# Optimization experiments

Hardware: AMD Instinct MI355X
Metric: run time of the kernel (lower is better)

Reference implementation:

```python
import jax, jax.numpy as jnp
import numpy as np

EPS = 1e-5      # BatchNorm eps (eval mode, running stats at init: mean=0, var=1)
SLOPE = 0.2     # LeakyReLU negative slope


def _knn_idx(x, k):
    # x: (B, N, D) -> (B, N, k) indices of k nearest neighbors (squared L2, feature space)
    sq = jnp.sum(x * x, axis=-1)                              # (B, N)
    dist = sq[:, :, None] + sq[:, None, :] - 2.0 * jnp.einsum('bnd,bmd->bnm', x, x)
    return jax.lax.top_k(-dist, k)[1]                         # nearest = largest of -dist


def _bn_lrelu(y, gamma, beta):
    # eval BatchNorm with running_mean=0, running_var=1, then LeakyReLU(0.2)
    y = y * (gamma / jnp.sqrt(1.0 + EPS)) + beta
    return jnp.where(y >= 0, y, SLOPE * y)


def _edge_conv(x, W, gamma, beta, k):
    # x: (B, N, D); W: (C_out, 2D). Returns (B, N, C_out) after max over k neighbors.
    idx = _knn_idx(x, k)                                      # (B, N, k)
    nb = jax.vmap(lambda xt, i: xt[i])(x, idx)                # (B, N, k, D) neighbor gather
    ctr = jnp.broadcast_to(x[:, :, None, :], nb.shape)
    feat = jnp.concatenate([nb - ctr, ctr], axis=-1)          # (B, N, k, 2D)
    y = jnp.einsum('bnkd,od->bnko', feat, W)                  # 1x1 conv (no bias)
    y = _bn_lrelu(y, gamma, beta)
    return jnp.max(y, axis=2)                                 # max-pool over neighbors


def setup_inputs() -> dict:
    key = jax.random.key(0)
    ks = jax.random.split(key, 16)
    B, N, k, out_dim = 8, 4096, 20, 512
    x = jax.random.normal(ks[0], (B, 3, N), dtype=jnp.float32)
    dims = [(64, 6), (64, 128), (128, 128), (256, 256), (out_dim, 512)]
    inp = {'x': x, 'k': k}
    for i, (co, ci) in enumerate(dims, start=1):
        inp[f'W{i}'] = jax.random.normal(ks[3 * i - 2], (co, ci), dtype=jnp.float32) * (1.0 / np.sqrt(ci))
        inp[f'g{i}'] = jax.random.uniform(ks[3 * i - 1], (co,), dtype=jnp.float32, minval=0.5, maxval=1.5)
        inp[f'b{i}'] = 0.1 * jax.random.normal(ks[3 * i], (co,), dtype=jnp.float32)
    return inp


def reference(x, W1, g1, b1, W2, g2, b2, W3, g3, b3, W4, g4, b4, W5, g5, b5, k):
    xt = jnp.transpose(x, (0, 2, 1))                          # (B, N, 3)
    x1 = _edge_conv(xt, W1, g1, b1, k)                        # (B, N, 64)
    x2 = _edge_conv(x1, W2, g2, b2, k)                        # (B, N, 64)
    x3 = _edge_conv(x2, W3, g3, b3, k)                        # (B, N, 128)
    x4 = _edge_conv(x3, W4, g4, b4, k)                        # (B, N, 256)
    h = jnp.concatenate([x1, x2, x3, x4], axis=-1)            # (B, N, 512)
    y = _bn_lrelu(jnp.einsum('bnd,od->bno', h, W5), g5, b5)   # (B, N, out_dim)
    return jnp.concatenate([jnp.max(y, axis=1), jnp.mean(y, axis=1)], axis=-1)  # (B, 2*out_dim)
```

## Files before the change

### kernel.cpp

```cpp
#include <hip/hip_runtime.h>
#include <math.h>

#define BATCH 8
#define N_PTS 4096
#define KNN 20
#define EPS_BN 1e-5f
#define SLOPE 0.2f
#define M_ROWS (BATCH * N_PTS)

typedef __attribute__((ext_vector_type(8))) short short8;
typedef __attribute__((ext_vector_type(2))) float float2v;
typedef __attribute__((ext_vector_type(4))) float float4v;
typedef __attribute__((ext_vector_type(16))) float float16v;

__device__ __forceinline__ unsigned short f2bf(float f) {
    unsigned u = __float_as_uint(f);
    unsigned r = (u + 0x7FFFu + ((u >> 16) & 1u)) >> 16;
    return (unsigned short)r;
}
__device__ __forceinline__ float bf2f(unsigned short h) {
    return __uint_as_float((unsigned)h << 16);
}

__global__ void convert_x1(const float* __restrict__ x,
                           unsigned short* __restrict__ xh, unsigned short* __restrict__ xl,
                           float* __restrict__ sq) {
    int i = blockIdx.x * blockDim.x + threadIdx.x;
    if (i >= M_ROWS) return;
    int b = i / N_PTS, n = i % N_PTS;
    float v[3], s = 0.f;
    #pragma unroll
    for (int d = 0; d < 3; ++d) {
        v[d] = x[((size_t)b * 3 + d) * N_PTS + n];
        s += v[d] * v[d];
    }
    sq[i] = s;
    #pragma unroll
    for (int d = 0; d < 32; ++d) {
        float f = (d < 3) ? v[d] : 0.f;
        unsigned short h = f2bf(f);
        xh[(size_t)i * 32 + d] = h;
        xl[(size_t)i * 32 + d] = f2bf(f - bf2f(h));
    }
}

__global__ void sqnorm_hl(const unsigned short* __restrict__ hh,
                          const unsigned short* __restrict__ hl,
                          int D, float* __restrict__ sq) {
    int w = threadIdx.x >> 6, lane = threadIdx.x & 63;
    int row = blockIdx.x * 4 + w;
    if (row >= M_ROWS) return;
    const unsigned short* ph = hh + (size_t)row * 512;
    const unsigned short* pl = hl + (size_t)row * 512;
    float s = 0.f;
    for (int d = lane; d < D; d += 64) {
        float v = bf2f(ph[d]) + bf2f(pl[d]);
        s += v * v;
    }
    #pragma unroll
    for (int off = 32; off > 0; off >>= 1) s += __shfl_down(s, off, 64);
    if (lane == 0) sq[row] = s;
}

__global__ void repack_edge_split(const float* __restrict__ W, int Co, int D, int KP,
                                  unsigned short* __restrict__ Wh, unsigned short* __restrict__ Wl) {
    int i = blockIdx.x * blockDim.x + threadIdx.x;
    int tot = 2 * Co * KP;
    if (i >= tot) return;
    int r = i / KP, d = i % KP;
    float v = 0.f;
    if (d < D) v = (r < Co) ? W[(size_t)r * 2 * D + d] : W[(size_t)(r - Co) * 2 * D + D + d];
    unsigned short h = f2bf(v);
    Wh[i] = h; Wl[i] = f2bf(v - bf2f(h));
}

__global__ void repack_w5_split(const float* __restrict__ W,
                                unsigned short* __restrict__ Wh, unsigned short* __restrict__ Wl) {
    int i = blockIdx.x * blockDim.x + threadIdx.x;
    if (i >= 512 * 512) return;
    float v = W[i];
    unsigned short h = f2bf(v);
    Wh[i] = h; Wl[i] = f2bf(v - bf2f(h));
}

template<int DPAD>
__launch_bounds__(DPAD >= 128 ? 256 : 512, 2)
__global__ void knn_mfma(const unsigned short* __restrict__ Xh,
                         const unsigned short* __restrict__ Xl,
                         int strideX,
                         const float* __restrict__ sq, int* __restrict__ idxout) {
    constexpr int KS16 = DPAD / 16;
    constexpr int NW   = (DPAD >= 128) ? 4 : 8;
    constexpr int NCH  = NW / 4;
    constexpr int CHR  = N_PTS / NCH;
    constexpr int SST  = 34;
    constexpr size_t SFB   = (size_t)NW * 32 * SST * 4;
    constexpr size_t THR   = (size_t)NW * 64 * 4;
    constexpr size_t MERGE = (size_t)64 * NW * KNN * 4 + (size_t)64 * NW * KNN * 2;
    constexpr size_t POOL  = (SFB + THR) > MERGE ? (SFB + THR) : MERGE;
    __shared__ __align__(16) char smem[POOL];
    float* Sfw  = (float*)smem + (size_t)(threadIdx.x >> 6) * 32 * SST;
    float* thrT = (float*)(smem + SFB);
    float*          kb   = (float*)smem;
    unsigned short* ib16 = (unsigned short*)(kb + 64 * NW * KNN);

    const int b = blockIdx.y;
    const int row0 = blockIdx.x * 64;
    const int tid = threadIdx.x;
    const int w = tid >> 6, lane = tid & 63;
    const int l31 = lane & 31, lh = lane >> 5;
    const int rbase = (w & 1) * 32;
    const int cb32  = ((w >> 1) & 1) * 32;
    const int chalf = w >> 2;
    const int cs    = chalf * CHR;
    const int rowb  = rbase + l31;
    const int slot  = ((w >> 1) & 1) * 2 + lh + chalf * 4;

    const unsigned short* Xhb = Xh + (size_t)b * N_PTS * strideX;
    const unsigned short* Xlb = Xl + (size_t)b * N_PTS * strideX;
    const float* sqb = sq + (size_t)b * N_PTS;

    short8 ah[KS16], al[KS16];
    #pragma unroll
    for (int ks = 0; ks < KS16; ++ks) {
        size_t o = (size_t)(row0 + rbase + l31) * strideX + ks * 16 + lh * 8;
        ah[ks] = *(const short8*)(Xhb + o);
        al[ks] = *(const short8*)(Xlb + o);
    }

    const unsigned short* pBh = Xhb + (size_t)(cb32 + l31) * strideX + lh * 8;
    const unsigned short* pBl = Xlb + (size_t)(cb32 + l31) * strideX + lh * 8;
    const float* psq = sqb + cb32 + l31;

    float fv[KNN]; int fi[KNN];
    #pragma unroll
    for (int p = 0; p < KNN; ++p) { fv[p] = INFINITY; fi[p] = 0x7FFFFFFF; }

    thrT[tid] = INFINITY;
    __syncthreads();

    #pragma unroll 1
    for (int c0 = cs; c0 < cs + CHR; c0 += 64) {
        short8 bh[KS16], bl[KS16];
        #pragma unroll
        for (int ks = 0; ks < KS16; ++ks) {
            bh[ks] = *(const short8*)(pBh + (size_t)c0 * strideX + ks * 16);
            bl[ks] = *(const short8*)(pBl + (size_t)c0 * strideX + ks * 16);
        }
        float sc = psq[c0];

        float16v a0 = {}, a1 = {}, a2 = {};
        #pragma unroll
        for (int ks = 0; ks < KS16; ++ks) {
            if (KS16 <= 4) {
                a0 = __builtin_amdgcn_mfma_f32_32x32x16_bf16(ah[ks], bh[ks], a0, 0, 0, 0);
                a1 = __builtin_amdgcn_mfma_f32_32x32x16_bf16(al[ks], bh[ks], a1, 0, 0, 0);
                a2 = __builtin_amdgcn_mfma_f32_32x32x16_bf16(ah[ks], bl[ks], a2, 0, 0, 0);
            } else {
                a0 = __builtin_amdgcn_mfma_f32_32x32x16_bf16(ah[ks], bh[ks], a0, 0, 0, 0);
                a1 = __builtin_amdgcn_mfma_f32_32x32x16_bf16(al[ks], bh[ks], a1, 0, 0, 0);
                a0 = __builtin_amdgcn_mfma_f32_32x32x16_bf16(ah[ks], bl[ks], a0, 0, 0, 0);
            }
        }

        #pragma unroll
        for (int reg = 0; reg < 16; ++reg) {
            int rowL = (reg & 3) + 8 * (reg >> 2) + 4 * lh;
            float acv = (KS16 <= 4) ? (a0[reg] + a1[reg] + a2[reg]) : (a0[reg] + a1[reg]);
            Sfw[rowL * SST + l31] = sc - 2.f * acv;
        }
        asm volatile("s_waitcnt lgkmcnt(0)" ::: "memory");

        float fT = thrT[rowb];
        #pragma unroll
        for (int s = 1; s < NW; ++s) fT = fminf(fT, thrT[s * 64 + rowb]);
        float f19 = fv[KNN - 1];

        const int sbase = l31 * SST + lh * 16;
        float2v c2[8];
        #pragma unroll
        for (int u = 0; u < 8; ++u) c2[u] = *(const float2v*)&Sfw[sbase + 2 * u];
        unsigned mask = 0;
        #pragma unroll
        for (int u = 0; u < 8; ++u) {
            if (c2[u][0] < f19 && c2[u][0] <= fT) mask |= (1u << (2 * u));
            if (c2[u][1] < f19 && c2[u][1] <= fT) mask |= (1u << (2 * u + 1));
        }

        const int cidx = c0 + cb32 + lh * 16;
        while (mask) {
            int jj = __ffs(mask) - 1;
            mask &= mask - 1;
            bool j1 = jj & 1, j2 = jj & 2, j4 = jj & 4, j8 = jj & 8;
            float t0 = j1 ? c2[0][1] : c2[0][0];
            float t1 = j1 ? c2[1][1] : c2[1][0];
            float t2 = j1 ? c2[2][1] : c2[2][0];
            float t3 = j1 ? c2[3][1] : c2[3][0];
            float t4 = j1 ? c2[4][1] : c2[4][0];
            float t5 = j1 ? c2[5][1] : c2[5][0];
            float t6 = j1 ? c2[6][1] : c2[6][0];
            float t7 = j1 ? c2[7][1] : c2[7][0];
            float u0 = j2 ? t1 : t0;
            float u1 = j2 ? t3 : t2;
            float u2 = j2 ? t5 : t4;
            float u3 = j2 ? t7 : t6;
            float r0 = j4 ? u1 : u0;
            float r1 = j4 ? u3 : u2;
            float v  = j8 ? r1 : r0;
            if (v < fv[KNN - 1]) {
                fv[KNN - 1] = v;
                fi[KNN - 1] = cidx + jj;
                #pragma unroll
                for (int p = KNN - 1; p > 0; --p) {
                    float va = fv[p - 1], vb = fv[p];
                    int   ia = fi[p - 1], ic = fi[p];
                    bool sw = vb < va;
                    fv[p - 1] = sw ? vb : va; fv[p] = sw ? va : vb;
                    fi[p - 1] = sw ? ic : ia; fi[p] = sw ? ia : ic;
                }
            }
        }

        thrT[slot * 64 + rowb] = fv[KNN - 1];
    }

    __syncthreads();
    {
        int base = (rowb * NW + slot) * KNN;
        #pragma unroll
        for (int p = 0; p < KNN; ++p) {
            kb[base + p] = fv[p];
            ib16[base + p] = (unsigned short)fi[p];
        }
    }
    __syncthreads();

    if constexpr (NW == 8) {
        if (tid < 128) {
            int row = tid & 63, half = tid >> 6;
            int base = (row * 8 + half * 4) * KNN;
            #pragma unroll
            for (int p = 0; p < KNN; ++p) { fv[p] = kb[base + p]; fi[p] = (int)ib16[base + p]; }
            #pragma unroll 1
            for (int qq = 0; qq < 3 * KNN; ++qq) {
                float v  = kb[base + KNN + qq];
                int   ii = (int)ib16[base + KNN + qq];
                bool ins = (v < fv[KNN - 1]) ||
                           (v == fv[KNN - 1] && ii < fi[KNN - 1]);
                if (ins) {
                    fv[KNN - 1] = v; fi[KNN - 1] = ii;
                    #pragma unroll
                    for (int p = KNN - 1; p > 0; --p) {
                        float va = fv[p - 1], vb = fv[p];
                        int   ia = fi[p - 1], ic = fi[p];
                        bool sw = (vb < va) || (vb == va && ic < ia);
                        fv[p - 1] = sw ? vb : va; fv[p] = sw ? va : vb;
                        fi[p - 1] = sw ? ic : ia; fi[p] = sw ? ia : ic;
                    }
                }
            }
            if (half == 1) {
                int ob = (row * 8 + 4) * KNN;
                #pragma unroll
                for (int p = 0; p < KNN; ++p) {
                    kb[ob + p] = fv[p]; ib16[ob + p] = (unsigned short)fi[p];
                }
            }
        }
        __syncthreads();
        if (tid < 64) {
            int base = (tid * 8 + 4) * KNN;
            #pragma unroll 1
            for (int qq = 0; qq < KNN; ++qq) {
                float v  = kb[base + qq];
                int   ii = (int)ib16[base + qq];
                bool ins = (v < fv[KNN - 1]) ||
                           (v == fv[KNN - 1] && ii < fi[KNN - 1]);
                if (ins) {
                    fv[KNN - 1] = v; fi[KNN - 1] = ii;
                    #pragma unroll
                    for (int p = KNN - 1; p > 0; --p) {
                        float va = fv[p - 1], vb = fv[p];
                        int   ia = fi[p - 1], ic = fi[p];
                        bool sw = (vb < va) || (vb == va && ic < ia);
                        fv[p - 1] = sw ? vb : va; fv[p] = sw ? va : vb;
                        fi[p - 1] = sw ? ic : ia; fi[p] = sw ? ia : ic;
                    }
                }
            }
            int* op = idxout + ((size_t)(b * N_PTS + row0 + tid)) * KNN;
            #pragma unroll
            for (int p = 0; p < KNN; ++p) op[p] = fi[p];
        }
    } else {
        if (tid < 64) {
            int base = tid * 4 * KNN;
            #pragma unroll
            for (int p = 0; p < KNN; ++p) { fv[p] = kb[base + p]; fi[p] = (int)ib16[base + p]; }
            #pragma unroll 1
            for (int qq = 0; qq < 3 * KNN; ++qq) {
                float v  = kb[base + KNN + qq];
                int   ii = (int)ib16[base + KNN + qq];
                bool ins = (v < fv[KNN - 1]) ||
                           (v == fv[KNN - 1] && ii < fi[KNN - 1]);
                if (ins) {
                    fv[KNN - 1] = v; fi[KNN - 1] = ii;
                    #pragma unroll
                    for (int p = KNN - 1; p > 0; --p) {
                        float va = fv[p - 1], vb = fv[p];
                        int   ia = fi[p - 1], ic = fi[p];
                        bool sw = (vb < va) || (vb == va && ic < ia);
                        fv[p - 1] = sw ? vb : va; fv[p] = sw ? va : vb;
                        fi[p - 1] = sw ? ic : ia; fi[p] = sw ? ia : ic;
                    }
                }
            }
            int* op = idxout + ((size_t)(b * N_PTS + row0 + tid)) * KNN;
            #pragma unroll
            for (int p = 0; p < KNN; ++p) op[p] = fi[p];
        }
    }
}

__launch_bounds__(256)
__global__ void fgemm(const unsigned short* __restrict__ Ah, const unsigned short* __restrict__ Al,
                      int strideA, int K,
                      const unsigned short* __restrict__ Wh, const unsigned short* __restrict__ Wl,
                      int C, float* __restrict__ out, int fuse_bn,
                      const float* __restrict__ g, const float* __restrict__ beta) {
    __shared__ unsigned short AhS[128 * 40];
    __shared__ unsigned short AlS[128 * 40];
    __shared__ unsigned short BhS[128 * 40];
    __shared__ unsigned short BlS[128 * 40];

    const int c0 = blockIdx.x * 128;
    const int m0 = blockIdx.y * 128;
    const int tid = threadIdx.x;
    const int w = tid >> 6, lane = tid & 63;
    const int n = lane & 15, q = lane >> 4;

    float4v acc[2][8];
    #pragma unroll
    for (int rt = 0; rt < 2; ++rt)
        #pragma unroll
        for (int ct = 0; ct < 8; ++ct) acc[rt][ct] = (float4v){0.f, 0.f, 0.f, 0.f};

    for (int kk = 0; kk < K; kk += 32) {
        __syncthreads();
        for (int tt = tid; tt < 512; tt += 256) {
            int rr = tt >> 2, c8 = tt & 3;
            size_t oa = (size_t)(m0 + rr) * strideA + kk + c8 * 8;
            *(short8*)&AhS[rr * 40 + c8 * 8] = *(const short8*)(Ah + oa);
            *(short8*)&AlS[rr * 40 + c8 * 8] = *(const short8*)(Al + oa);
            size_t ob = (size_t)(c0 + rr) * K + kk + c8 * 8;
            *(short8*)&BhS[rr * 40 + c8 * 8] = *(const short8*)(Wh + ob);
            *(short8*)&BlS[rr * 40 + c8 * 8] = *(const short8*)(Wl + ob);
        }
        __syncthreads();

        short8 af[2][2];
        #pragma unroll
        for (int rt = 0; rt < 2; ++rt) {
            af[rt][0] = *(const short8*)&AhS[(w * 32 + rt * 16 + n) * 40 + q * 8];
            af[rt][1] = *(const short8*)&AlS[(w * 32 + rt * 16 + n) * 40 + q * 8];
        }
        #pragma unroll
        for (int ct = 0; ct < 8; ++ct) {
            short8 bh = *(const short8*)&BhS[(ct * 16 + n) * 40 + q * 8];
            short8 bl = *(const short8*)&BlS[(ct * 16 + n) * 40 + q * 8];
            #pragma unroll
            for (int rt = 0; rt < 2; ++rt) {
                acc[rt][ct] = __builtin_amdgcn_mfma_f32_16x16x32_bf16(af[rt][0], bh, acc[rt][ct], 0, 0, 0);
                acc[rt][ct] = __builtin_amdgcn_mfma_f32_16x16x32_bf16(af[rt][1], bh, acc[rt][ct], 0, 0, 0);
                acc[rt][ct] = __builtin_amdgcn_mfma_f32_16x16x32_bf16(af[rt][0], bl, acc[rt][ct], 0, 0, 0);
            }
        }
    }

    #pragma unroll
    for (int rt = 0; rt < 2; ++rt)
        #pragma unroll
        for (int ct = 0; ct < 8; ++ct) {
            int c = c0 + ct * 16 + n;
            float sc = 1.f, bt = 0.f;
            if (fuse_bn) { sc = g[c] / sqrtf(1.f + EPS_BN); bt = beta[c]; }
            #pragma unroll
            for (int e = 0; e < 4; ++e) {
                int m = m0 + w * 32 + rt * 16 + q * 4 + e;
                float v = acc[rt][ct][e];
                if (fuse_bn) { v = v * sc + bt; v = (v >= 0.f) ? v : SLOPE * v; }
                out[(size_t)m * C + c] = v;
            }
        }
}

__global__ void pool_kernel(const float* __restrict__ zc2, int Co,
                            const int* __restrict__ idx,
                            const float* __restrict__ g, const float* __restrict__ beta,
                            unsigned short* __restrict__ hh, unsigned short* __restrict__ hl,
                            int hoff) {
    int n = blockIdx.x, b = blockIdx.y;
    int o = threadIdx.x;
    size_t bn = (size_t)b * N_PTS + n;
    const int* ip = idx + bn * KNN;
    float zn   = zc2[bn * (size_t)(2 * Co) + o];
    float base = zc2[bn * (size_t)(2 * Co) + Co + o] - zn;
    float m = -INFINITY;
    #pragma unroll
    for (int j = 0; j < KNN; ++j) {
        size_t rr = (size_t)b * N_PTS + ip[j];
        m = fmaxf(m, zc2[rr * (size_t)(2 * Co) + o]);
    }
    float y = m + base;
    float sc = g[o] / sqrtf(1.f + EPS_BN);
    y = y * sc + beta[o];
    y = (y >= 0.f) ? y : SLOPE * y;
    unsigned short h = f2bf(y);
    hh[bn * 512 + hoff + o] = h;
    hl[bn * 512 + hoff + o] = f2bf(y - bf2f(h));
}

__global__ void reduce_partial(const float* __restrict__ y5,
                               float* __restrict__ pmax, float* __restrict__ psum) {
    int chunk = blockIdx.x, b = blockIdx.y, c = threadIdx.x;
    float mx = -INFINITY, sm = 0.f;
    for (int qq = 0; qq < 128; ++qq) {
        int n = chunk * 128 + qq;
        float v = y5[((size_t)b * N_PTS + n) * 512 + c];
        mx = fmaxf(mx, v);
        sm += v;
    }
    pmax[((size_t)b * 32 + chunk) * 512 + c] = mx;
    psum[((size_t)b * 32 + chunk) * 512 + c] = sm;
}

__global__ void reduce_final(const float* __restrict__ pmax,
                             const float* __restrict__ psum,
                             float* __restrict__ out) {
    int i = blockIdx.x * blockDim.x + threadIdx.x;
    if (i >= BATCH * 512) return;
    int b = i / 512, c = i % 512;
    float mx = -INFINITY, sm = 0.f;
    for (int qq = 0; qq < 32; ++qq) {
        mx = fmaxf(mx, pmax[((size_t)b * 32 + qq) * 512 + c]);
        sm += psum[((size_t)b * 32 + qq) * 512 + c];
    }
    out[(size_t)b * 1024 + c] = mx;
    out[(size_t)b * 1024 + 512 + c] = sm * (1.f / 4096.f);
}

extern "C" void kernel_launch(void* const* d_in, const int* in_sizes, int n_in,
                              void* d_out, int out_size, void* d_ws, size_t ws_size,
                              hipStream_t stream) {
    const float* x = (const float*)d_in[0];
    const float* W[5], *gg[5], *bb[5];
    for (int i = 0; i < 5; ++i) {
        W[i]  = (const float*)d_in[2 + 3 * i];
        gg[i] = (const float*)d_in[3 + 3 * i];
        bb[i] = (const float*)d_in[4 + 3 * i];
    }
    float* outp = (float*)d_out;

    char* wsb = (char*)d_ws;
    size_t off = 0;
    unsigned short* x1h = (unsigned short*)(wsb + off); off += (size_t)M_ROWS * 32 * 2;
    unsigned short* x1l = (unsigned short*)(wsb + off); off += (size_t)M_ROWS * 32 * 2;
    float* sq = (float*)(wsb + off); off += (size_t)M_ROWS * 4;
    int*   idx = (int*)(wsb + off); off += (size_t)M_ROWS * KNN * 4;
    unsigned short* Wh = (unsigned short*)(wsb + off); off += (size_t)512 * 512 * 2;
    unsigned short* Wl = (unsigned short*)(wsb + off); off += (size_t)512 * 512 * 2;
    unsigned short* hh = (unsigned short*)(wsb + off); off += (size_t)M_ROWS * 512 * 2;
    unsigned short* hl = (unsigned short*)(wsb + off); off += (size_t)M_ROWS * 512 * 2;
    float* zc2 = (float*)(wsb + off); off += (size_t)M_ROWS * 512 * 4;
    float* pmx = (float*)(wsb + off); off += (size_t)BATCH * 32 * 512 * 4;
    float* psm = (float*)(wsb + off); off += (size_t)BATCH * 32 * 512 * 4;
    (void)ws_size; (void)in_sizes; (void)n_in; (void)out_size;

    convert_x1<<<(M_ROWS + 255) / 256, 256, 0, stream>>>(x, x1h, x1l, sq);

    struct L { int D, Co, KP, hoff; };
    const L layers[4] = { {3, 64, 32, 0}, {64, 64, 64, 64}, {64, 128, 64, 128}, {128, 256, 128, 256} };

    for (int li = 0; li < 4; ++li) {
        const L& ly = layers[li];
        const unsigned short* Ahp;
        const unsigned short* Alp;
        int strideA;
        if (li == 0) { Ahp = x1h; Alp = x1l; strideA = 32; }
        else {
            int po = layers[li - 1].hoff;
            Ahp = hh + po; Alp = hl + po; strideA = 512;
            sqnorm_hl<<<M_ROWS / 4, 256, 0, stream>>>(Ahp, Alp, ly.D, sq);
        }

        if (li == 0)
            knn_mfma<32><<<dim3(N_PTS / 64, BATCH), 512, 0, stream>>>(Ahp, Alp, strideA, sq, idx);
        else if (ly.D == 64)
            knn_mfma<64><<<dim3(N_PTS / 64, BATCH), 512, 0, stream>>>(Ahp, Alp, strideA, sq, idx);
        else
            knn_mfma<128><<<dim3(N_PTS / 64, BATCH), 256, 0, stream>>>(Ahp, Alp, strideA, sq, idx);

        repack_edge_split<<<(2 * ly.Co * ly.KP + 255) / 256, 256, 0, stream>>>(
            W[li], ly.Co, ly.D, ly.KP, Wh, Wl);
        fgemm<<<dim3((2 * ly.Co) / 128, M_ROWS / 128), 256, 0, stream>>>(
            Ahp, Alp, strideA, ly.KP, Wh, Wl, 2 * ly.Co, zc2, 0, nullptr, nullptr);
        pool_kernel<<<dim3(N_PTS, BATCH), ly.Co, 0, stream>>>(
            zc2, ly.Co, idx, gg[li], bb[li], hh, hl, ly.hoff);
    }

    repack_w5_split<<<(512 * 512 + 255) / 256, 256, 0, stream>>>(W[4], Wh, Wl);
    fgemm<<<dim3(4, M_ROWS / 128), 256, 0, stream>>>(
        hh, hl, 512, 512, Wh, Wl, 512, zc2, 1, gg[4], bb[4]);

    reduce_partial<<<dim3(32, BATCH), 512, 0, stream>>>(zc2, pmx, psm);
    reduce_final<<<(BATCH * 512 + 255) / 256, 256, 0, stream>>>(pmx, psm, outp);
}
```

Baseline: 1.778 ms.

## Restructure kNN kernel to 32-row blocks with 8 column-slice lists per row

Each kNN block now handles 32 query rows with 4 waves, each wave striding over column tiles of 32, so each row keeps 8 partial top-k lists merged in two stages. The grid doubles and launch bounds allow more blocks per CU. For small D the third MFMA accumulator is dropped and the split-bf16 correction terms are summed into one accumulator. The aim is better occupancy and load balance in the kNN pass, at the cost of less reuse of each loaded column tile across rows and a heavier per-row merge.

```diff
diff --git a/kernel.cpp b/kernel.cpp
--- a/kernel.cpp
+++ b/kernel.cpp
@@ -84,37 +84,30 @@
 }
 
 template<int DPAD>
-__launch_bounds__(DPAD >= 128 ? 256 : 512, 2)
+__launch_bounds__(256, DPAD >= 128 ? 2 : 4)
 __global__ void knn_mfma(const unsigned short* __restrict__ Xh,
                          const unsigned short* __restrict__ Xl,
                          int strideX,
                          const float* __restrict__ sq, int* __restrict__ idxout) {
     constexpr int KS16 = DPAD / 16;
-    constexpr int NW   = (DPAD >= 128) ? 4 : 8;
-    constexpr int NCH  = NW / 4;
-    constexpr int CHR  = N_PTS / NCH;
     constexpr int SST  = 34;
-    constexpr size_t SFB   = (size_t)NW * 32 * SST * 4;
-    constexpr size_t THR   = (size_t)NW * 64 * 4;
-    constexpr size_t MERGE = (size_t)64 * NW * KNN * 4 + (size_t)64 * NW * KNN * 2;
+    constexpr size_t SFB   = (size_t)4 * 32 * SST * 4;
+    constexpr size_t THR   = (size_t)256 * 4;
+    constexpr size_t MERGE = (size_t)32 * 8 * KNN * 4 + (size_t)32 * 8 * KNN * 2;
     constexpr size_t POOL  = (SFB + THR) > MERGE ? (SFB + THR) : MERGE;
     __shared__ __align__(16) char smem[POOL];
     float* Sfw  = (float*)smem + (size_t)(threadIdx.x >> 6) * 32 * SST;
     float* thrT = (float*)(smem + SFB);
     float*          kb   = (float*)smem;
-    unsigned short* ib16 = (unsigned short*)(kb + 64 * NW * KNN);
+    unsigned short* ib16 = (unsigned short*)(kb + 32 * 8 * KNN);
 
     const int b = blockIdx.y;
-    const int row0 = blockIdx.x * 64;
+    const int row0 = blockIdx.x * 32;
     const int tid = threadIdx.x;
     const int w = tid >> 6, lane = tid & 63;
     const int l31 = lane & 31, lh = lane >> 5;
-    const int rbase = (w & 1) * 32;
-    const int cb32  = ((w >> 1) & 1) * 32;
-    const int chalf = w >> 2;
-    const int cs    = chalf * CHR;
-    const int rowb  = rbase + l31;
-    const int slot  = ((w >> 1) & 1) * 2 + lh + chalf * 4;
+    const int rowb = l31;
+    const int slot = w * 2 + lh;
 
     const unsigned short* Xhb = Xh + (size_t)b * N_PTS * strideX;
     const unsigned short* Xlb = Xl + (size_t)b * N_PTS * strideX;
@@ -123,14 +116,14 @@
     short8 ah[KS16], al[KS16];
     #pragma unroll
     for (int ks = 0; ks < KS16; ++ks) {
-        size_t o = (size_t)(row0 + rbase + l31) * strideX + ks * 16 + lh * 8;
+        size_t o = (size_t)(row0 + l31) * strideX + ks * 16 + lh * 8;
         ah[ks] = *(const short8*)(Xhb + o);
         al[ks] = *(const short8*)(Xlb + o);
     }
 
-    const unsigned short* pBh = Xhb + (size_t)(cb32 + l31) * strideX + lh * 8;
-    const unsigned short* pBl = Xlb + (size_t)(cb32 + l31) * strideX + lh * 8;
-    const float* psq = sqb + cb32 + l31;
+    const unsigned short* pBh = Xhb + (size_t)l31 * strideX + lh * 8;
+    const unsigned short* pBl = Xlb + (size_t)l31 * strideX + lh * 8;
+    const float* psq = sqb + l31;
 
     float fv[KNN]; int fi[KNN];
     #pragma unroll
@@ -140,7 +133,8 @@
     __syncthreads();
 
     #pragma unroll 1
-    for (int c0 = cs; c0 < cs + CHR; c0 += 64) {
+    for (int t = 0; t < 32; ++t) {
+        const int c0 = w * 32 + t * 128;
         short8 bh[KS16], bl[KS16];
         #pragma unroll
         for (int ks = 0; ks < KS16; ++ks) {
@@ -149,31 +143,25 @@
         }
         float sc = psq[c0];
 
-        float16v a0 = {}, a1 = {}, a2 = {};
+        float16v a0 = {}, a1 = {};
         #pragma unroll
         for (int ks = 0; ks < KS16; ++ks) {
-            if (KS16 <= 4) {
-                a0 = __builtin_amdgcn_mfma_f32_32x32x16_bf16(ah[ks], bh[ks], a0, 0, 0, 0);
-                a1 = __builtin_amdgcn_mfma_f32_32x32x16_bf16(al[ks], bh[ks], a1, 0, 0, 0);
-                a2 = __builtin_amdgcn_mfma_f32_32x32x16_bf16(ah[ks], bl[ks], a2, 0, 0, 0);
-            } else {
-                a0 = __builtin_amdgcn_mfma_f32_32x32x16_bf16(ah[ks], bh[ks], a0, 0, 0, 0);
-                a1 = __builtin_amdgcn_mfma_f32_32x32x16_bf16(al[ks], bh[ks], a1, 0, 0, 0);
-                a0 = __builtin_amdgcn_mfma_f32_32x32x16_bf16(ah[ks], bl[ks], a0, 0, 0, 0);
-            }
+            a0 = __builtin_amdgcn_mfma_f32_32x32x16_bf16(ah[ks], bh[ks], a0, 0, 0, 0);
+            a1 = __builtin_amdgcn_mfma_f32_32x32x16_bf16(al[ks], bh[ks], a1, 0, 0, 0);
+            a0 = __builtin_amdgcn_mfma_f32_32x32x16_bf16(ah[ks], bl[ks], a0, 0, 0, 0);
         }
 
         #pragma unroll
         for (int reg = 0; reg < 16; ++reg) {
             int rowL = (reg & 3) + 8 * (reg >> 2) + 4 * lh;
-            float acv = (KS16 <= 4) ? (a0[reg] + a1[reg] + a2[reg]) : (a0[reg] + a1[reg]);
-            Sfw[rowL * SST + l31] = sc - 2.f * acv;
+            Sfw[rowL * SST + l31] = sc - 2.f * (a0[reg] + a1[reg]);
         }
         asm volatile("s_waitcnt lgkmcnt(0)" ::: "memory");
 
-        float fT = thrT[rowb];
-        #pragma unroll
-        for (int s = 1; s < NW; ++s) fT = fminf(fT, thrT[s * 64 + rowb]);
+        float fT = fminf(fminf(fminf(thrT[rowb],       thrT[32 + rowb]),
+                               fminf(thrT[64 + rowb],  thrT[96 + rowb])),
+                         fminf(fminf(thrT[128 + rowb], thrT[160 + rowb]),
+                               fminf(thrT[192 + rowb], thrT[224 + rowb])));
         float f19 = fv[KNN - 1];
 
         const int sbase = l31 * SST + lh * 16;
@@ -187,7 +175,7 @@
             if (c2[u][1] < f19 && c2[u][1] <= fT) mask |= (1u << (2 * u + 1));
         }
 
-        const int cidx = c0 + cb32 + lh * 16;
+        const int cidx = c0 + lh * 16;
         while (mask) {
             int jj = __ffs(mask) - 1;
             mask &= mask - 1;
@@ -221,12 +209,12 @@
             }
         }
 
-        thrT[slot * 64 + rowb] = fv[KNN - 1];
+        thrT[slot * 32 + rowb] = fv[KNN - 1];
     }
 
     __syncthreads();
     {
-        int base = (rowb * NW + slot) * KNN;
+        int base = (rowb * 8 + slot) * KNN;
         #pragma unroll
         for (int p = 0; p < KNN; ++p) {
             kb[base + p] = fv[p];
@@ -235,90 +223,61 @@
     }
     __syncthreads();
 
-    if constexpr (NW == 8) {
-        if (tid < 128) {
-            int row = tid & 63, half = tid >> 6;
-            int base = (row * 8 + half * 4) * KNN;
+    if (tid < 64) {
+        int row = tid & 31, half = tid >> 5;
+        int base = (row * 8 + half * 4) * KNN;
+        #pragma unroll
+        for (int p = 0; p < KNN; ++p) { fv[p] = kb[base + p]; fi[p] = (int)ib16[base + p]; }
+        #pragma unroll 1
+        for (int qq = 0; qq < 3 * KNN; ++qq) {
+            float v  = kb[base + KNN + qq];
+            int   ii = (int)ib16[base + KNN + qq];
+            bool ins = (v < fv[KNN - 1]) ||
+                       (v == fv[KNN - 1] && ii < fi[KNN - 1]);
+            if (ins) {
+                fv[KNN - 1] = v; fi[KNN - 1] = ii;
+                #pragma unroll
+                for (int p = KNN - 1; p > 0; --p) {
+                    float va = fv[p - 1], vb = fv[p];
+                    int   ia = fi[p - 1], ic = fi[p];
+                    bool sw = (vb < va) || (vb == va && ic < ia);
+                    fv[p - 1] = sw ? vb : va; fv[p] = sw ? va : vb;
+                    fi[p - 1] = sw ? ic : ia; fi[p] = sw ? ia : ic;
+                }
+            }
+        }
+        if (half == 1) {
+            int ob = (row * 8 + 4) * KNN;
             #pragma unroll
-            for (int p = 0; p < KNN; ++p) { fv[p] = kb[base + p]; fi[p] = (int)ib16[base + p]; }
-            #pragma unroll 1
-            for (int qq = 0; qq < 3 * KNN; ++qq) {
-                float v  = kb[base + KNN + qq];
-                int   ii = (int)ib16[base + KNN + qq];
-                bool ins = (v < fv[KNN - 1]) ||
-                           (v == fv[KNN - 1] && ii < fi[KNN - 1]);
-                if (ins) {
-                    fv[KNN - 1] = v; fi[KNN - 1] = ii;
-                    #pragma unroll
-                    for (int p = KNN - 1; p > 0; --p) {
-                        float va = fv[p - 1], vb = fv[p];
-                        int   ia = fi[p - 1], ic = fi[p];
-                        bool sw = (vb < va) || (vb == va && ic < ia);
-                        fv[p - 1] = sw ? vb : va; fv[p] = sw ? va : vb;
-                        fi[p - 1] = sw ? ic : ia; fi[p] = sw ? ia : ic;
-                    }
+            for (int p = 0; p < KNN; ++p) {
+                kb[ob + p] = fv[p]; ib16[ob + p] = (unsigned short)fi[p];
+            }
+        }
+    }
+    __syncthreads();
+    if (tid < 32) {
+        int base = (tid * 8 + 4) * KNN;
+        #pragma unroll 1
+        for (int qq = 0; qq < KNN; ++qq) {
+            float v  = kb[base + qq];
+            int   ii = (int)ib16[base + qq];
+            bool ins = (v < fv[KNN - 1]) ||
+                       (v == fv[KNN - 1] && ii < fi[KNN - 1]);
+            if (ins) {
+                fv[KNN - 1] = v; fi[KNN - 1] = ii;
+                #pragma unroll
+                for (int p = KNN - 1; p > 0; --p) {
+                    float va = fv[p - 1], vb = fv[p];
+                    int   ia = fi[p - 1], ic = fi[p];
+                    bool sw = (vb < va) || (vb == va && ic < ia);
+                    fv[p - 1] = sw ? vb : va; fv[p] = sw ? va : vb;
+                    fi[p - 1] = sw ? ic : ia; fi[p] = sw ? ia : ic;
                 }
             }
-            if (half == 1) {
-                int ob = (row * 8 + 4) * KNN;
-                #pragma unroll
-                for (int p = 0; p < KNN; ++p) {
-                    kb[ob + p] = fv[p]; ib16[ob + p] = (unsigned short)fi[p];
-                }
-            }
-        }
-        __syncthreads();
-        if (tid < 64) {
-            int base = (tid * 8 + 4) * KNN;
-            #pragma unroll 1
-            for (int qq = 0; qq < KNN; ++qq) {
-                float v  = kb[base + qq];
-                int   ii = (int)ib16[base + qq];
-                bool ins = (v < fv[KNN - 1]) ||
-                           (v == fv[KNN - 1] && ii < fi[KNN - 1]);
-                if (ins) {
-                    fv[KNN - 1] = v; fi[KNN - 1] = ii;
-                    #pragma unroll
-                    for (int p = KNN - 1; p > 0; --p) {
-                        float va = fv[p - 1], vb = fv[p];
-                        int   ia = fi[p - 1], ic = fi[p];
-                        bool sw = (vb < va) || (vb == va && ic < ia);
-                        fv[p - 1] = sw ? vb : va; fv[p] = sw ? va : vb;
-                        fi[p - 1] = sw ? ic : ia; fi[p] = sw ? ia : ic;
-                    }
-                }
-            }
-            int* op = idxout + ((size_t)(b * N_PTS + row0 + tid)) * KNN;
-            #pragma unroll
-            for (int p = 0; p < KNN; ++p) op[p] = fi[p];
-        }
-    } else {
-        if (tid < 64) {
-            int base = tid * 4 * KNN;
-            #pragma unroll
-            for (int p = 0; p < KNN; ++p) { fv[p] = kb[base + p]; fi[p] = (int)ib16[base + p]; }
-            #pragma unroll 1
-            for (int qq = 0; qq < 3 * KNN; ++qq) {
-                float v  = kb[base + KNN + qq];
-                int   ii = (int)ib16[base + KNN + qq];
-                bool ins = (v < fv[KNN - 1]) ||
-                           (v == fv[KNN - 1] && ii < fi[KNN - 1]);
-                if (ins) {
-                    fv[KNN - 1] = v; fi[KNN - 1] = ii;
-                    #pragma unroll
-                    for (int p = KNN - 1; p > 0; --p) {
-                        float va = fv[p - 1], vb = fv[p];
-                        int   ia = fi[p - 1], ic = fi[p];
-                        bool sw = (vb < va) || (vb == va && ic < ia);
-                        fv[p - 1] = sw ? vb : va; fv[p] = sw ? va : vb;
-                        fi[p - 1] = sw ? ic : ia; fi[p] = sw ? ia : ic;
-                    }
-                }
-            }
-            int* op = idxout + ((size_t)(b * N_PTS + row0 + tid)) * KNN;
-            #pragma unroll
-            for (int p = 0; p < KNN; ++p) op[p] = fi[p];
-        }
+        }
+        int* op = idxout + ((size_t)(b * N_PTS + row0 + tid)) * KNN;
+        #pragma unroll
+        for (int p = 0; p < KNN; ++p) op[p] = fi[p];
     }
 }
 
@@ -494,11 +453,11 @@
         }
 
         if (li == 0)
-            knn_mfma<32><<<dim3(N_PTS / 64, BATCH), 512, 0, stream>>>(Ahp, Alp, strideA, sq, idx);
+            knn_mfma<32><<<dim3(N_PTS / 32, BATCH), 256, 0, stream>>>(Ahp, Alp, strideA, sq, idx);
         else if (ly.D == 64)
-            knn_mfma<64><<<dim3(N_PTS / 64, BATCH), 512, 0, stream>>>(Ahp, Alp, strideA, sq, idx);
+            knn_mfma<64><<<dim3(N_PTS / 32, BATCH), 256, 0, stream>>>(Ahp, Alp, strideA, sq, idx);
         else
-            knn_mfma<128><<<dim3(N_PTS / 64, BATCH), 256, 0, stream>>>(Ahp, Alp, strideA, sq, idx);
+            knn_mfma<128><<<dim3(N_PTS / 32, BATCH), 256, 0, stream>>>(Ahp, Alp, strideA, sq, idx);
 
         repack_edge_split<<<(2 * ly.Co * ly.KP + 255) / 256, 256, 0, stream>>>(
             W[li], ly.Co, ly.D, ly.KP, Wh, Wl);
```

After: 1.659 ms. -6.7%, faster.
